# Optimization experiments

Measured on AMD Instinct MI355X. Metric: run time of the kernel, lower is better.

The kernel has to match this reference:

```python
import jax, jax.numpy as jnp
import numpy as np

E = 1024      # emb_size == hidden_size
H = 8         # n_heads
BATCH = 8
NUM = 48      # table rows
KW = 48       # table columns (keys)
L = NUM * KW  # 2304


def _mha(q_in, kv_in, length, Wq, bq, Wk, bk, Wv, bv, Wo, bo, n_heads=H):
    # q_in: (B, T, E), kv_in: (B, S, E); returns (T, B, E) per the torch layout.
    B, T, Em = q_in.shape
    S = kv_in.shape[1]
    dh = Em // n_heads
    q = (q_in @ Wq + bq).reshape(B, T, n_heads, dh).transpose(0, 2, 1, 3)
    k = (kv_in @ Wk + bk).reshape(B, S, n_heads, dh).transpose(0, 2, 1, 3)
    v = (kv_in @ Wv + bv).reshape(B, S, n_heads, dh).transpose(0, 2, 1, 3)
    scores = jnp.einsum('bhtd,bhsd->bhts', q, k) / jnp.asarray(np.sqrt(dh), q.dtype)
    mask = jnp.arange(S) < length  # memory_lengths masking
    scores = jnp.where(mask[None, None, None, :], scores, jnp.finfo(scores.dtype).min)
    attn = jax.nn.softmax(scores, axis=-1)
    out = jnp.einsum('bhts,bhsd->bhtd', attn, v).transpose(0, 2, 1, 3).reshape(B, T, Em)
    out = out @ Wo + bo
    return out.transpose(1, 0, 2)  # (T, B, E)


def setup_inputs() -> dict:
    key = jax.random.key(0)
    ks = jax.random.split(key, 24)

    def W(k, shape, s=0.03):
        return jax.random.normal(k, shape, dtype=jnp.float32) * s

    inp = {
        'emb': jax.random.normal(ks[0], (L, BATCH, E), dtype=jnp.float32),
        # col attention params
        'Wq_c': W(ks[1], (E, E)), 'bq_c': jnp.zeros((E,), jnp.float32),
        'Wk_c': W(ks[2], (E, E)), 'bk_c': jnp.zeros((E,), jnp.float32),
        'Wv_c': W(ks[3], (E, E)), 'bv_c': jnp.zeros((E,), jnp.float32),
        'Wo_c': W(ks[4], (E, E)), 'bo_c': jnp.zeros((E,), jnp.float32),
        # row attention params
        'Wq_r': W(ks[5], (E, E)), 'bq_r': jnp.zeros((E,), jnp.float32),
        'Wk_r': W(ks[6], (E, E)), 'bk_r': jnp.zeros((E,), jnp.float32),
        'Wv_r': W(ks[7], (E, E)), 'bv_r': jnp.zeros((E,), jnp.float32),
        'Wo_r': W(ks[8], (E, E)), 'bo_r': jnp.zeros((E,), jnp.float32),
        # fusion layers
        'W_gen': W(ks[9], (2 * E, E)),
        'W_mlp1': W(ks[10], (2 * E, E)),
        'W_mlp2': W(ks[11], (E, 1)),
        # scalar forward args
        'start_id': 0, 'end_id': L - 1,
        'num': NUM, 'num_tensor': NUM,
        'kw_num': KW, 'kw_num_tensor': KW,
        'batch': BATCH,
    }
    return inp


def reference(emb, Wq_c, bq_c, Wk_c, bk_c, Wv_c, bv_c, Wo_c, bo_c,
              Wq_r, bq_r, Wk_r, bk_r, Wv_r, bv_r, Wo_r, bo_r,
              W_gen, W_mlp1, W_mlp2,
              start_id, end_id, num, num_tensor, kw_num, kw_num_tensor, batch):
    Em = emb.shape[-1]
    length = end_id - start_id + 1  # = num * kw_num
    # emb.narrow(0, start_id, length): (L, batch, E)
    rep = emb[start_id:start_id + length]
    # -> (kw_num, batch*num, E)
    home_ply_rep = rep.transpose(1, 0, 2).reshape(batch * num, kw_num, Em).transpose(1, 0, 2)

    # --- column-dim encoding: attention over the `num` (row) axis ---
    col_mb = jnp.swapaxes(home_ply_rep.reshape(kw_num, batch, num, Em), 0, 2)  # (num, batch, kw, E)
    col_mb = col_mb.reshape(num, batch * kw_num, Em)
    col_q = col_mb.transpose(1, 0, 2)  # (batch*kw, num, E)
    col_rep = _mha(col_q, col_q, num_tensor, Wq_c, bq_c, Wk_c, bk_c, Wv_c, bv_c, Wo_c, bo_c)
    # (num, batch*kw, E) -> (kw_num, batch*num, E)
    col_dim_rep = jnp.swapaxes(col_rep.reshape(num, batch, kw_num, Em), 0, 2).reshape(kw_num, batch * num, Em)

    # --- row-dim encoding: attention over the `kw_num` (column) axis ---
    row_q = col_dim_rep.transpose(1, 0, 2)  # (batch*num, kw, E)
    row_dim_rep = _mha(row_q, row_q, kw_num_tensor, Wq_r, bq_r, Wk_r, bk_r, Wv_r, bv_r, Wo_r, bo_r)  # (kw, b*n, E)

    # --- fusion: concat + Linear + tanh, MLP scores, softmax over {row, col} ---
    gen_rep = jnp.tanh(jnp.concatenate([row_dim_rep, col_dim_rep], axis=-1) @ W_gen)

    def mlp_score(x):
        return jnp.tanh(jnp.concatenate([x, gen_rep], axis=-1) @ W_mlp1) @ W_mlp2  # (kw, b*n, 1)

    row_score = mlp_score(row_dim_rep)
    col_score = mlp_score(col_dim_rep)
    w = jax.nn.softmax(jnp.concatenate([row_score, col_score], axis=-1), axis=-1)  # (kw, b*n, 2)
    home_ply_memory_bank = w[..., 0:1] * row_dim_rep + w[..., 1:2] * col_dim_rep
    # no_fusion=True -> residual add
    home_ply_memory_bank = home_ply_memory_bank + home_ply_rep

    row_for_ptr = row_dim_rep.reshape(kw_num, batch, num, Em)
    col_for_ptr = col_dim_rep.reshape(kw_num, batch, num, Em)

    # row_aggregation == 'mean'
    home_ply_row_rep = home_ply_memory_bank.mean(axis=0)  # (batch*num, E)
    home_ply_row_rep = home_ply_row_rep.reshape(batch, num, Em).transpose(1, 0, 2)  # (num, batch, E)
    return (home_ply_row_rep, home_ply_memory_bank, col_for_ptr, row_for_ptr)
```

## Files before the change

kernel.cpp:

```cpp
#include <hip/hip_runtime.h>
#include <hip/hip_bf16.h>
#include <stdint.h>

typedef unsigned short u16;
typedef unsigned int   u32;
typedef __attribute__((ext_vector_type(4))) float f32x4;
typedef __attribute__((ext_vector_type(2))) float f32x2;
typedef __attribute__((ext_vector_type(8))) short s16x8;

#define DEV __device__ __forceinline__

static constexpr int EDIM  = 1024;
static constexpr int MROWS = 8 * 48 * 48;
static constexpr int MT256 = MROWS / 256;

DEV float b2f(u16 x) { u32 u = ((u32)x) << 16; float f; __builtin_memcpy(&f, &u, 4); return f; }
DEV u16 f2b(float f) {
    u32 u; __builtin_memcpy(&u, &f, 4);
    u32 r = (u + 0x7FFFu + ((u >> 16) & 1u)) >> 16;
    return (u16)r;
}

#define GLDS16(gsrc, ldst) __builtin_amdgcn_global_load_lds( \
    (const __attribute__((address_space(1))) u32*)(gsrc),    \
    (__attribute__((address_space(3))) u32*)(ldst), 16, 0, 0)

#define BAR()   __builtin_amdgcn_s_barrier()
#define LGKM0() asm volatile("s_waitcnt lgkmcnt(0)" ::: "memory")

__global__ void wconv_kernel(const float* __restrict__ W, u16* __restrict__ Wt,
                             int K, int N) {
    __shared__ u16 tile[64][65];
    int n0 = blockIdx.x * 64, k0 = blockIdx.y * 64;
    int tx = threadIdx.x & 63, ty = threadIdx.x >> 6;
#pragma unroll
    for (int i = 0; i < 16; ++i) {
        int r = ty * 16 + i;
        tile[r][tx] = f2b(W[(size_t)(k0 + r) * N + n0 + tx]);
    }
    __syncthreads();
#pragma unroll
    for (int i = 0; i < 16; ++i) {
        int r = ty * 16 + i;
        Wt[(size_t)(n0 + r) * K + k0 + tx] = tile[tx][r];
    }
}

__global__ void bconcat_kernel(const float* __restrict__ a, const float* __restrict__ b,
                               const float* __restrict__ c, float* __restrict__ out) {
    int i = blockIdx.x * 256 + threadIdx.x;
    out[i] = (i < 1024) ? a[i] : ((i < 2048) ? b[i - 1024] : c[i - 2048]);
}

__global__ void gather_kernel(const float* __restrict__ emb, u16* __restrict__ Xc) {
    int gid = blockIdx.x * 256 + threadIdx.x;
    int r = gid >> 9, c2 = gid & 511;
    int b = r / 2304, k = (r / 48) % 48, n = r % 48;
    int src = (n * 48 + k) * 8 + b;
    f32x2 v = *(const f32x2*)&emb[(size_t)src * EDIM + c2 * 2];
    u32 p = (u32)f2b(v.x) | ((u32)f2b(v.y) << 16);
    *(u32*)&Xc[(size_t)r * EDIM + c2 * 2] = p;
}

__global__ void zero_kernel(float* __restrict__ p, int n) {
    int i = blockIdx.x * 256 + threadIdx.x;
    if (i < n) p[i] = 0.f;
}

DEV s16x8 ldsrd(const u16* lds, int r, int kk, int qq) {
    int gl = kk * 4 + qq;
    return *(const s16x8*)&lds[r * 64 + ((gl ^ (r & 7)) << 3)];
}

DEV void stage_tileA(u16* lds, const u16* Ag, int lda, int m0, int ka,
                     int h, int wv, int lane) {
#pragma unroll
    for (int i = 0; i < 2; ++i) {
        int blk  = wv * 2 + i;
        int row0 = (h + 2 * (blk >> 3)) * 64 + (blk & 7) * 8;
        int rr   = row0 + (lane >> 3);
        int gl   = (lane & 7) ^ (rr & 7);
        const u16* g = Ag + (size_t)(m0 + rr) * lda + ka + gl * 8;
        GLDS16(g, lds + row0 * 64);
    }
}

DEV void stage_tileB(u16* lds, const u16* Bg, int ldb, int n0, int kb,
                     int h, int wv, int lane) {
#pragma unroll
    for (int i = 0; i < 2; ++i) {
        int blk  = wv * 2 + i;
        int row0 = (blk >> 2) * 64 + h * 32 + (blk & 3) * 8;
        int rr   = row0 + (lane >> 3);
        int gl   = (lane & 7) ^ (rr & 7);
        const u16* g = Bg + (size_t)(n0 + rr) * ldb + kb + gl * 8;
        GLDS16(g, lds + row0 * 64);
    }
}

template<int KTOT, bool DUALA, bool TANH, bool PERM, bool SCORE, bool WRC, int OMAP, bool MERGE2>
__global__ __launch_bounds__(512, 2) void gemm256_kernel(
    const u16* __restrict__ A1, const u16* __restrict__ A1b,
    const u16* __restrict__ A2, int lda,
    const u16* __restrict__ Bt, const float* __restrict__ bias,
    u16* __restrict__ C, int ldc, float* __restrict__ outF,
    const float* __restrict__ w2, float* __restrict__ score,
    float* __restrict__ scoreb) {
    __shared__ u16 lA[2][256 * 64];
    __shared__ u16 lB[2][256 * 64];
    constexpr int NT = KTOT / 64;

    int bid = blockIdx.x;
    if (MERGE2 && bid >= MT256 * 4) { bid -= MT256 * 4; A1 = A1b; score = scoreb; }
    int mt = bid % MT256, nt = bid / MT256;
    int m0 = mt * 256, n0 = nt * 256;
    int tid = threadIdx.x, lane = tid & 63, wv = tid >> 6;
    int wm = wv >> 2, wn = wv & 3;
    int fr = lane & 15, qq = lane >> 4;

    auto Asel = [&](int ts, const u16*& Ag, int& ka) {
        ka = ts * 64; Ag = A1;
        if (DUALA && ka >= 1024) { Ag = A2; ka -= 1024; }
    };

    f32x4 acc[8][4];
#pragma unroll
    for (int i = 0; i < 8; ++i)
#pragma unroll
        for (int j = 0; j < 4; ++j) acc[i][j] = (f32x4)0.f;

    {
        const u16* Ag; int ka; Asel(0, Ag, ka);
        stage_tileA(&lA[0][0], Ag, lda, m0, ka, 0, wv, lane);
        stage_tileA(&lA[0][0], Ag, lda, m0, ka, 1, wv, lane);
        stage_tileB(&lB[0][0], Bt, KTOT, n0, 0, 0, wv, lane);
        stage_tileB(&lB[0][0], Bt, KTOT, n0, 0, 1, wv, lane);
    }
    if (NT > 1) {
        const u16* Ag; int ka; Asel(1, Ag, ka);
        stage_tileA(&lA[1][0], Ag, lda, m0, ka, 0, wv, lane);
        stage_tileB(&lB[1][0], Bt, KTOT, n0, 64, 0, wv, lane);
        stage_tileB(&lB[1][0], Bt, KTOT, n0, 64, 1, wv, lane);
    }
    asm volatile("s_waitcnt vmcnt(6)" ::: "memory");
    BAR();

    s16x8 A8[8], B0[4], B1[4];

    for (int t = 0; t < NT; ++t) {
        int buf = t & 1;
        const u16* lAb = &lA[buf][0];
        const u16* lBb = &lB[buf][0];

#pragma unroll
        for (int m = 0; m < 4; ++m)
#pragma unroll
            for (int kk = 0; kk < 2; ++kk)
                A8[m * 2 + kk] = ldsrd(lAb, wm * 128 + m * 16 + fr, kk, qq);
#pragma unroll
        for (int n = 0; n < 2; ++n)
#pragma unroll
            for (int kk = 0; kk < 2; ++kk)
                B0[n * 2 + kk] = ldsrd(lBb, wn * 64 + n * 16 + fr, kk, qq);
        if (t + 1 < NT) {
            const u16* Ag; int ka; Asel(t + 1, Ag, ka);
            stage_tileA(&lA[buf ^ 1][0], Ag, lda, m0, ka, 1, wv, lane);
        }
        BAR(); LGKM0();
        __builtin_amdgcn_s_setprio(1);
#pragma unroll
        for (int m = 0; m < 4; ++m)
#pragma unroll
            for (int n = 0; n < 2; ++n)
#pragma unroll
                for (int kk = 0; kk < 2; ++kk)
                    acc[m][n] = __builtin_amdgcn_mfma_f32_16x16x32_bf16(
                        A8[m * 2 + kk], B0[n * 2 + kk], acc[m][n], 0, 0, 0);
        __builtin_amdgcn_s_setprio(0);
        BAR();

#pragma unroll
        for (int n = 0; n < 2; ++n)
#pragma unroll
            for (int kk = 0; kk < 2; ++kk)
                B1[n * 2 + kk] = ldsrd(lBb, wn * 64 + 32 + n * 16 + fr, kk, qq);
        if (t + 2 < NT) {
            const u16* Ag; int ka; Asel(t + 2, Ag, ka);
            stage_tileA(&lA[buf][0], Ag, lda, m0, ka, 0, wv, lane);
        }
        BAR(); LGKM0();
        __builtin_amdgcn_s_setprio(1);
#pragma unroll
        for (int m = 0; m < 4; ++m)
#pragma unroll
            for (int n = 0; n < 2; ++n)
#pragma unroll
                for (int kk = 0; kk < 2; ++kk)
                    acc[m][n + 2] = __builtin_amdgcn_mfma_f32_16x16x32_bf16(
                        A8[m * 2 + kk], B1[n * 2 + kk], acc[m][n + 2], 0, 0, 0);
        __builtin_amdgcn_s_setprio(0);
        BAR();

#pragma unroll
        for (int m = 0; m < 4; ++m)
#pragma unroll
            for (int kk = 0; kk < 2; ++kk)
                A8[m * 2 + kk] = ldsrd(lAb, wm * 128 + 64 + m * 16 + fr, kk, qq);
        if (t + 2 < NT)
            stage_tileB(&lB[buf][0], Bt, KTOT, n0, (t + 2) * 64, 0, wv, lane);
        BAR(); LGKM0();
        __builtin_amdgcn_s_setprio(1);
#pragma unroll
        for (int m = 0; m < 4; ++m)
#pragma unroll
            for (int n = 0; n < 2; ++n)
#pragma unroll
                for (int kk = 0; kk < 2; ++kk)
                    acc[m + 4][n] = __builtin_amdgcn_mfma_f32_16x16x32_bf16(
                        A8[m * 2 + kk], B0[n * 2 + kk], acc[m + 4][n], 0, 0, 0);
        __builtin_amdgcn_s_setprio(0);
        BAR();

        if (t + 2 < NT)
            stage_tileB(&lB[buf][0], Bt, KTOT, n0, (t + 2) * 64, 1, wv, lane);
        __builtin_amdgcn_s_setprio(1);
#pragma unroll
        for (int m = 0; m < 4; ++m)
#pragma unroll
            for (int n = 0; n < 2; ++n)
#pragma unroll
                for (int kk = 0; kk < 2; ++kk)
                    acc[m + 4][n + 2] = __builtin_amdgcn_mfma_f32_16x16x32_bf16(
                        A8[m * 2 + kk], B1[n * 2 + kk], acc[m + 4][n + 2], 0, 0, 0);
        __builtin_amdgcn_s_setprio(0);
        if (t < NT - 2)       asm volatile("s_waitcnt vmcnt(6)" ::: "memory");
        else if (t == NT - 2) asm volatile("s_waitcnt vmcnt(0)" ::: "memory");
        BAR();
    }

    int crow4 = qq * 4;
#pragma unroll
    for (int mf = 0; mf < 8; ++mf) {
#pragma unroll
        for (int j = 0; j < 4; ++j) {
            int row = m0 + wm * 128 + mf * 16 + crow4 + j;
            int orow = row;
            int o32 = 0;
            if (PERM || OMAP == 1) {
                int b = row / 2304, k = (row / 48) % 48, n = row % 48;
                if (PERM) orow = (b * 48 + n) * 48 + k;
                if (OMAP == 1) o32 = k * 384 + b * 48 + n;
            }
            if (OMAP == 2) {
                int b = row / 2304, n = (row / 48) % 48, k = row % 48;
                o32 = k * 384 + b * 48 + n;
            }
            float sc_part = 0.f;
#pragma unroll
            for (int nf = 0; nf < 4; ++nf) {
                int col = n0 + wn * 64 + nf * 16 + fr;
                float v = acc[mf][nf][j];
                if (bias) v += bias[col];
                if (TANH) v = tanhf(v);
                if (WRC) C[(size_t)orow * ldc + col] = f2b(v);
                if (OMAP) outF[(size_t)o32 * EDIM + col] = v;
                if (SCORE) sc_part += v * w2[col];
            }
            if (SCORE) {
                sc_part += __shfl_xor(sc_part, 1);
                sc_part += __shfl_xor(sc_part, 2);
                sc_part += __shfl_xor(sc_part, 4);
                sc_part += __shfl_xor(sc_part, 8);
                if (fr == 0) atomicAdd(&score[row], sc_part);
            }
        }
    }
}

__global__ __launch_bounds__(64) void attn_kernel(u16* __restrict__ QKV) {
    __shared__ u16 lVt[128 * 72];
    __shared__ u16 lP[48 * 72];
    const int LDQ = 3072;
    int bb = blockIdx.x >> 3, h = blockIdx.x & 7;
    int lane = threadIdx.x;
    u16* Qp = QKV + (size_t)bb * 48 * LDQ + h * 128;
    const u16* Kp = Qp + 1024;
    const u16* Vp = Qp + 2048;

#pragma unroll
    for (int i = 0; i < 48; ++i) {
        u32 vv = *(const u32*)&Vp[(size_t)i * LDQ + lane * 2];
        lVt[(lane * 2) * 72 + i]     = (u16)(vv & 0xffffu);
        lVt[(lane * 2 + 1) * 72 + i] = (u16)(vv >> 16);
    }
    for (int i = lane; i < 128 * 16; i += 64) { int d = i >> 4, c = 48 + (i & 15); lVt[d * 72 + c] = 0; }
    for (int i = lane; i < 48 * 16; i += 64)  { int t = i >> 4, c = 48 + (i & 15); lP[t * 72 + c] = 0; }
    __syncthreads();

    int fr = lane & 15, fk = (lane >> 4) * 8, crow4 = (lane >> 4) * 4;
    f32x4 sc[3][3];
#pragma unroll
    for (int mf = 0; mf < 3; ++mf)
#pragma unroll
        for (int nf = 0; nf < 3; ++nf) sc[mf][nf] = (f32x4)0.f;

#pragma unroll
    for (int kk = 0; kk < 4; ++kk) {
        s16x8 aq[3], bk[3];
#pragma unroll
        for (int mf = 0; mf < 3; ++mf) aq[mf] = *(const s16x8*)&Qp[(size_t)(mf * 16 + fr) * LDQ + kk * 32 + fk];
#pragma unroll
        for (int nf = 0; nf < 3; ++nf) bk[nf] = *(const s16x8*)&Kp[(size_t)(nf * 16 + fr) * LDQ + kk * 32 + fk];
#pragma unroll
        for (int mf = 0; mf < 3; ++mf)
#pragma unroll
            for (int nf = 0; nf < 3; ++nf)
                sc[mf][nf] = __builtin_amdgcn_mfma_f32_16x16x32_bf16(aq[mf], bk[nf], sc[mf][nf], 0, 0, 0);
    }

    const float scale = 0.08838834764831845f;
#pragma unroll
    for (int mf = 0; mf < 3; ++mf) {
#pragma unroll
        for (int j = 0; j < 4; ++j) {
            float v0 = sc[mf][0][j] * scale;
            float v1 = sc[mf][1][j] * scale;
            float v2 = sc[mf][2][j] * scale;
            float mx = fmaxf(v0, fmaxf(v1, v2));
            mx = fmaxf(mx, __shfl_xor(mx, 1));
            mx = fmaxf(mx, __shfl_xor(mx, 2));
            mx = fmaxf(mx, __shfl_xor(mx, 4));
            mx = fmaxf(mx, __shfl_xor(mx, 8));
            float e0 = __expf(v0 - mx), e1 = __expf(v1 - mx), e2 = __expf(v2 - mx);
            float s = e0 + e1 + e2;
            s += __shfl_xor(s, 1);
            s += __shfl_xor(s, 2);
            s += __shfl_xor(s, 4);
            s += __shfl_xor(s, 8);
            float inv = 1.f / s;
            int t = mf * 16 + crow4 + j;
            lP[t * 72 + 0  + fr] = f2b(e0 * inv);
            lP[t * 72 + 16 + fr] = f2b(e1 * inv);
            lP[t * 72 + 32 + fr] = f2b(e2 * inv);
        }
    }
    __syncthreads();

    f32x4 o[3][8];
#pragma unroll
    for (int mf = 0; mf < 3; ++mf)
#pragma unroll
        for (int nf = 0; nf < 8; ++nf) o[mf][nf] = (f32x4)0.f;

#pragma unroll
    for (int kk = 0; kk < 2; ++kk) {
        s16x8 ap[3];
#pragma unroll
        for (int mf = 0; mf < 3; ++mf) ap[mf] = *(const s16x8*)&lP[(mf * 16 + fr) * 72 + kk * 32 + fk];
#pragma unroll
        for (int nf = 0; nf < 8; ++nf) {
            s16x8 bv = *(const s16x8*)&lVt[(nf * 16 + fr) * 72 + kk * 32 + fk];
#pragma unroll
            for (int mf = 0; mf < 3; ++mf)
                o[mf][nf] = __builtin_amdgcn_mfma_f32_16x16x32_bf16(ap[mf], bv, o[mf][nf], 0, 0, 0);
        }
    }
#pragma unroll
    for (int mf = 0; mf < 3; ++mf)
#pragma unroll
        for (int nf = 0; nf < 8; ++nf)
#pragma unroll
            for (int j = 0; j < 4; ++j) {
                int t = mf * 16 + crow4 + j, d = nf * 16 + fr;
                Qp[(size_t)t * LDQ + d] = f2b(o[mf][nf][j]);
            }
}

__global__ void combine_kernel(const u16* __restrict__ RDR, const u16* __restrict__ CDR,
                               const float* __restrict__ srow, const float* __restrict__ scol,
                               const float* __restrict__ emb, float* __restrict__ out_mb) {
    int o = blockIdx.x;
    int k = o / 384, b = (o / 48) & 7, n = o % 48;
    int r2 = (b * 48 + n) * 48 + k;
    float rs = srow[r2], cs = scol[r2];
    float m = fmaxf(rs, cs);
    float e0 = __expf(rs - m), e1 = __expf(cs - m);
    float inv = 1.f / (e0 + e1);
    float w0 = e0 * inv, w1 = e1 * inv;
    const size_t rb = (size_t)r2 * EDIM;
    const size_t ob = (size_t)o * EDIM;
    const size_t eb = ((size_t)(n * 48 + k) * 8 + b) * EDIM;
    for (int e = threadIdx.x; e < EDIM; e += 256) {
        float rv = b2f(RDR[rb + e]);
        float cv = b2f(CDR[rb + e]);
        out_mb[ob + e] = w0 * rv + w1 * cv + emb[eb + e];
    }
}

__global__ void mean_kernel(const float* __restrict__ mb, float* __restrict__ out0) {
    int idx = blockIdx.x * 256 + threadIdx.x;
    int n = idx >> 13, b = (idx >> 10) & 7, e = idx & 1023;
    float s = 0.f;
#pragma unroll 8
    for (int k = 0; k < 48; ++k) s += mb[((size_t)(k * 384 + b * 48 + n)) * EDIM + e];
    out0[idx] = s * (1.f / 48.f);
}

extern "C" void kernel_launch(void* const* d_in, const int* in_sizes, int n_in,
                              void* d_out, int out_size, void* d_ws, size_t ws_size,
                              hipStream_t stream) {
    const float* emb    = (const float*)d_in[0];
    const float* Wq_c   = (const float*)d_in[1];
    const float* bq_c   = (const float*)d_in[2];
    const float* Wk_c   = (const float*)d_in[3];
    const float* bk_c   = (const float*)d_in[4];
    const float* Wv_c   = (const float*)d_in[5];
    const float* bv_c   = (const float*)d_in[6];
    const float* Wo_c   = (const float*)d_in[7];
    const float* bo_c   = (const float*)d_in[8];
    const float* Wq_r   = (const float*)d_in[9];
    const float* bq_r   = (const float*)d_in[10];
    const float* Wk_r   = (const float*)d_in[11];
    const float* bk_r   = (const float*)d_in[12];
    const float* Wv_r   = (const float*)d_in[13];
    const float* bv_r   = (const float*)d_in[14];
    const float* Wo_r   = (const float*)d_in[15];
    const float* bo_r   = (const float*)d_in[16];
    const float* W_gen  = (const float*)d_in[17];
    const float* W_mlp1 = (const float*)d_in[18];
    const float* W_mlp2 = (const float*)d_in[19];

    char* ws = (char*)d_ws;
    size_t off = 0;
    auto alloc = [&](size_t bytes) { char* p = ws + off; off += (bytes + 255) & ~(size_t)255; return p; };
    u16*   WqkvC = (u16*)alloc((size_t)3072 * 1024 * 2);
    u16*   WqkvR = (u16*)alloc((size_t)3072 * 1024 * 2);
    u16*   WoC   = (u16*)alloc((size_t)1024 * 1024 * 2);
    u16*   WoR   = (u16*)alloc((size_t)1024 * 1024 * 2);
    u16*   WgT   = (u16*)alloc((size_t)1024 * 2048 * 2);
    u16*   W1T   = (u16*)alloc((size_t)1024 * 2048 * 2);
    float* bqkvC = (float*)alloc(3072 * 4);
    float* bqkvR = (float*)alloc(3072 * 4);
    u16*   XA    = (u16*)alloc((size_t)MROWS * 1024 * 2);
    u16*   QKV   = (u16*)alloc((size_t)MROWS * 3072 * 2);
    u16*   CDR   = (u16*)alloc((size_t)MROWS * 1024 * 2);
    u16*   RDR   = (u16*)alloc((size_t)MROWS * 1024 * 2);
    float* score_row = (float*)alloc((size_t)MROWS * 4);
    float* score_col = (float*)alloc((size_t)MROWS * 4);
    (void)ws_size; (void)in_sizes; (void)n_in; (void)out_size;

    dim3 tb(256);
    wconv_kernel<<<dim3(16, 16), tb, 0, stream>>>(Wq_c, WqkvC,                   1024, 1024);
    wconv_kernel<<<dim3(16, 16), tb, 0, stream>>>(Wk_c, WqkvC + 1024 * 1024,     1024, 1024);
    wconv_kernel<<<dim3(16, 16), tb, 0, stream>>>(Wv_c, WqkvC + 2 * 1024 * 1024, 1024, 1024);
    wconv_kernel<<<dim3(16, 16), tb, 0, stream>>>(Wo_c, WoC,                     1024, 1024);
    wconv_kernel<<<dim3(16, 16), tb, 0, stream>>>(Wq_r, WqkvR,                   1024, 1024);
    wconv_kernel<<<dim3(16, 16), tb, 0, stream>>>(Wk_r, WqkvR + 1024 * 1024,     1024, 1024);
    wconv_kernel<<<dim3(16, 16), tb, 0, stream>>>(Wv_r, WqkvR + 2 * 1024 * 1024, 1024, 1024);
    wconv_kernel<<<dim3(16, 16), tb, 0, stream>>>(Wo_r, WoR,                     1024, 1024);
    wconv_kernel<<<dim3(16, 32), tb, 0, stream>>>(W_gen,  WgT, 2048, 1024);
    wconv_kernel<<<dim3(16, 32), tb, 0, stream>>>(W_mlp1, W1T, 2048, 1024);
    bconcat_kernel<<<12, tb, 0, stream>>>(bq_c, bk_c, bv_c, bqkvC);
    bconcat_kernel<<<12, tb, 0, stream>>>(bq_r, bk_r, bv_r, bqkvR);

    gather_kernel<<<MROWS * 512 / 256, tb, 0, stream>>>(emb, XA);
    zero_kernel<<<(2 * MROWS + 255) / 256, tb, 0, stream>>>(score_row, 2 * MROWS);

    float* out = (float*)d_out;
    float* out_mb  = out + 393216;
    float* out_col = out + 393216 + 18874368;
    float* out_row = out + 393216 + 2 * 18874368;

    dim3 tb512(512);
    const int G12 = MT256 * 12, G4 = MT256 * 4, G8m = MT256 * 8;
    gemm256_kernel<1024, false, false, false, false, true, 0, false><<<G12, tb512, 0, stream>>>(
        XA, nullptr, nullptr, 1024, WqkvC, bqkvC, QKV, 3072, nullptr, nullptr, nullptr, nullptr);
    attn_kernel<<<384 * 8, 64, 0, stream>>>(QKV);
    gemm256_kernel<1024, false, false, true, false, true, 1, false><<<G4, tb512, 0, stream>>>(
        QKV, nullptr, nullptr, 3072, WoC, bo_c, CDR, 1024, out_col, nullptr, nullptr, nullptr);
    gemm256_kernel<1024, false, false, false, false, true, 0, false><<<G12, tb512, 0, stream>>>(
        CDR, nullptr, nullptr, 1024, WqkvR, bqkvR, QKV, 3072, nullptr, nullptr, nullptr, nullptr);
    attn_kernel<<<384 * 8, 64, 0, stream>>>(QKV);
    gemm256_kernel<1024, false, false, false, false, true, 2, false><<<G4, tb512, 0, stream>>>(
        QKV, nullptr, nullptr, 3072, WoR, bo_r, RDR, 1024, out_row, nullptr, nullptr, nullptr);
    gemm256_kernel<2048, true, true, false, false, true, 0, false><<<G4, tb512, 0, stream>>>(
        RDR, nullptr, CDR, 1024, WgT, nullptr, XA, 1024, nullptr, nullptr, nullptr, nullptr);
    gemm256_kernel<2048, true, true, false, true, false, 0, true><<<G8m, tb512, 0, stream>>>(
        RDR, CDR, XA, 1024, W1T, nullptr, nullptr, 1024, nullptr, W_mlp2, score_row, score_col);

    combine_kernel<<<MROWS, tb, 0, stream>>>(RDR, CDR, score_row, score_col, emb, out_mb);
    mean_kernel<<<393216 / 256, tb, 0, stream>>>(out_mb, out);
}
```

Baseline: 1.203 ms.

## Fold output projections into downstream weights and persist GEMM tiles across jobs

Precomputes the products of the column-attention output projection with the row QKV weights, and of the row output projection with the first half of the gen weights, including folded biases. The row QKV projection and the gen GEMM can then read the attention outputs directly and run alongside the output-projection GEMMs in one persistent multi-job GEMM launch. The GEMM becomes a persistent 256-block kernel that prefetches the next tile's K-slices across tile boundaries and drops some barriers. Weight conversions, bias concatenation and score zeroing are batched into fewer launches, and combine plus mean are fused. The extra weight-product GEMMs run on every call, and products formed in bf16 add rounding error.

Measured after the change: 1.319 ms. +9.7%, slower.

```diff
diff --git a/kernel.cpp b/kernel.cpp
--- a/kernel.cpp
+++ b/kernel.cpp
@@ -12,7 +12,6 @@
 
 static constexpr int EDIM  = 1024;
 static constexpr int MROWS = 8 * 48 * 48;
-static constexpr int MT256 = MROWS / 256;
 
 DEV float b2f(u16 x) { u32 u = ((u32)x) << 16; float f; __builtin_memcpy(&f, &u, 4); return f; }
 DEV u16 f2b(float f) {
@@ -28,28 +27,89 @@
 #define BAR()   __builtin_amdgcn_s_barrier()
 #define LGKM0() asm volatile("s_waitcnt lgkmcnt(0)" ::: "memory")
 
-__global__ void wconv_kernel(const float* __restrict__ W, u16* __restrict__ Wt,
-                             int K, int N) {
+enum { F_WRC = 1, F_PERM = 2, F_TANH = 4, F_SCORE = 8, F_OMAP1 = 16, F_OMAP2 = 32 };
+
+struct GJob {
+    const u16* A1; const u16* A2; const u16* Bt; const float* bias;
+    u16* C; float* outF; const float* w2; float* score;
+    int lda, lda2, ldc, KTOT, M, flags, tileEnd, pad;
+};
+struct GSet { int njobs, total; GJob j[2]; };
+
+struct WJob { const float* src; u16* dst; int srcN, dstLd, kOff, nT, tileEnd, pad; };
+struct WSet { int n, total; WJob j[11]; };
+
+__global__ void wconvJ_kernel(WSet ws) {
+    int bid = blockIdx.x;
+    int ji = 0;
+    while (bid >= ws.j[ji].tileEnd) ++ji;
+    int base = ji ? ws.j[ji - 1].tileEnd : 0;
+    WJob J = ws.j[ji];
+    int lt = bid - base;
+    int n0 = (lt % J.nT) * 64, k0 = (lt / J.nT) * 64;
     __shared__ u16 tile[64][65];
-    int n0 = blockIdx.x * 64, k0 = blockIdx.y * 64;
     int tx = threadIdx.x & 63, ty = threadIdx.x >> 6;
 #pragma unroll
     for (int i = 0; i < 16; ++i) {
         int r = ty * 16 + i;
-        tile[r][tx] = f2b(W[(size_t)(k0 + r) * N + n0 + tx]);
+        tile[r][tx] = f2b(J.src[(size_t)(k0 + r) * J.srcN + n0 + tx]);
     }
     __syncthreads();
 #pragma unroll
     for (int i = 0; i < 16; ++i) {
         int r = ty * 16 + i;
-        Wt[(size_t)(n0 + r) * K + k0 + tx] = tile[tx][r];
-    }
-}
-
-__global__ void bconcat_kernel(const float* __restrict__ a, const float* __restrict__ b,
-                               const float* __restrict__ c, float* __restrict__ out) {
-    int i = blockIdx.x * 256 + threadIdx.x;
-    out[i] = (i < 1024) ? a[i] : ((i < 2048) ? b[i - 1024] : c[i - 2048]);
+        J.dst[(size_t)(n0 + r) * J.dstLd + J.kOff + k0 + tx] = tile[tx][r];
+    }
+}
+
+__global__ void misc_kernel(const float* WoCsrc, const float* WoRsrc,
+                            u16* WoCnt, u16* WoRnt,
+                            const float* bq_c, const float* bk_c, const float* bv_c, float* bqkvC,
+                            const float* bq_r, const float* bk_r, const float* bv_r,
+                            const float* bo_c, const u16* WqkvRT, float* bqkvR_eff,
+                            const float* bo_r, const u16* WgaT, float* bgen_lin,
+                            float* scores) {
+    int id = blockIdx.x * 256 + threadIdx.x;
+    const int C1 = 1024 * 1024 / 2;
+    if (id < C1) {
+        f32x2 v = *(const f32x2*)&WoCsrc[(size_t)id * 2];
+        *(u32*)&WoCnt[(size_t)id * 2] = (u32)f2b(v.x) | ((u32)f2b(v.y) << 16);
+        return;
+    }
+    id -= C1;
+    if (id < C1) {
+        f32x2 v = *(const f32x2*)&WoRsrc[(size_t)id * 2];
+        *(u32*)&WoRnt[(size_t)id * 2] = (u32)f2b(v.x) | ((u32)f2b(v.y) << 16);
+        return;
+    }
+    id -= C1;
+    if (id < 3072) { bqkvC[id] = (id < 1024) ? bq_c[id] : (id < 2048) ? bk_c[id - 1024] : bv_c[id - 2048]; return; }
+    id -= 3072;
+    if (id < 2 * MROWS) { scores[id] = 0.f; return; }
+    id -= 2 * MROWS;
+    if (id < 3072) {
+        float s = (id < 1024) ? bq_r[id] : (id < 2048) ? bk_r[id - 1024] : bv_r[id - 2048];
+        float d = 0.f;
+        const u16* row = &WqkvRT[(size_t)id * 1024];
+        for (int e = 0; e < 1024; e += 8) {
+            s16x8 v = *(const s16x8*)&row[e];
+#pragma unroll
+            for (int u = 0; u < 8; ++u) d += bo_c[e + u] * b2f((u16)v[u]);
+        }
+        bqkvR_eff[id] = s + d;
+        return;
+    }
+    id -= 3072;
+    if (id < 1024) {
+        float d = 0.f;
+        const u16* row = &WgaT[(size_t)id * 1024];
+        for (int e = 0; e < 1024; e += 8) {
+            s16x8 v = *(const s16x8*)&row[e];
+#pragma unroll
+            for (int u = 0; u < 8; ++u) d += bo_r[e + u] * b2f((u16)v[u]);
+        }
+        bgen_lin[id] = d;
+    }
 }
 
 __global__ void gather_kernel(const float* __restrict__ emb, u16* __restrict__ Xc) {
@@ -58,97 +118,91 @@
     int b = r / 2304, k = (r / 48) % 48, n = r % 48;
     int src = (n * 48 + k) * 8 + b;
     f32x2 v = *(const f32x2*)&emb[(size_t)src * EDIM + c2 * 2];
-    u32 p = (u32)f2b(v.x) | ((u32)f2b(v.y) << 16);
-    *(u32*)&Xc[(size_t)r * EDIM + c2 * 2] = p;
-}
-
-__global__ void zero_kernel(float* __restrict__ p, int n) {
-    int i = blockIdx.x * 256 + threadIdx.x;
-    if (i < n) p[i] = 0.f;
+    *(u32*)&Xc[(size_t)r * EDIM + c2 * 2] = (u32)f2b(v.x) | ((u32)f2b(v.y) << 16);
 }
 
 DEV s16x8 ldsrd(const u16* lds, int r, int kk, int qq) {
     int gl = kk * 4 + qq;
     return *(const s16x8*)&lds[r * 64 + ((gl ^ (r & 7)) << 3)];
 }
-
-DEV void stage_tileA(u16* lds, const u16* Ag, int lda, int m0, int ka,
-                     int h, int wv, int lane) {
+DEV void stageA_p(u16* lds, const u16* Ag, int lda, int m0, int ka, int h, int wv, int lane) {
 #pragma unroll
     for (int i = 0; i < 2; ++i) {
-        int blk  = wv * 2 + i;
+        int blk = wv * 2 + i;
         int row0 = (h + 2 * (blk >> 3)) * 64 + (blk & 7) * 8;
-        int rr   = row0 + (lane >> 3);
-        int gl   = (lane & 7) ^ (rr & 7);
-        const u16* g = Ag + (size_t)(m0 + rr) * lda + ka + gl * 8;
-        GLDS16(g, lds + row0 * 64);
-    }
-}
-
-DEV void stage_tileB(u16* lds, const u16* Bg, int ldb, int n0, int kb,
-                     int h, int wv, int lane) {
+        int rr = row0 + (lane >> 3);
+        int gl = (lane & 7) ^ (rr & 7);
+        GLDS16(Ag + (size_t)(m0 + rr) * lda + ka + gl * 8, lds + row0 * 64);
+    }
+}
+DEV void stageB_p(u16* lds, const u16* Bg, int ldb, int n0, int kb, int h, int wv, int lane) {
 #pragma unroll
     for (int i = 0; i < 2; ++i) {
-        int blk  = wv * 2 + i;
+        int blk = wv * 2 + i;
         int row0 = (blk >> 2) * 64 + h * 32 + (blk & 3) * 8;
-        int rr   = row0 + (lane >> 3);
-        int gl   = (lane & 7) ^ (rr & 7);
-        const u16* g = Bg + (size_t)(n0 + rr) * ldb + kb + gl * 8;
-        GLDS16(g, lds + row0 * 64);
-    }
-}
-
-template<int KTOT, bool DUALA, bool TANH, bool PERM, bool SCORE, bool WRC, int OMAP, bool MERGE2>
-__global__ __launch_bounds__(512, 2) void gemm256_kernel(
-    const u16* __restrict__ A1, const u16* __restrict__ A1b,
-    const u16* __restrict__ A2, int lda,
-    const u16* __restrict__ Bt, const float* __restrict__ bias,
-    u16* __restrict__ C, int ldc, float* __restrict__ outF,
-    const float* __restrict__ w2, float* __restrict__ score,
-    float* __restrict__ scoreb) {
+        int rr = row0 + (lane >> 3);
+        int gl = (lane & 7) ^ (rr & 7);
+        GLDS16(Bg + (size_t)(n0 + rr) * ldb + kb + gl * 8, lds + row0 * 64);
+    }
+}
+
+__global__ __launch_bounds__(512, 2) void gemmP_kernel(GSet js) {
     __shared__ u16 lA[2][256 * 64];
     __shared__ u16 lB[2][256 * 64];
-    constexpr int NT = KTOT / 64;
-
-    int bid = blockIdx.x;
-    if (MERGE2 && bid >= MT256 * 4) { bid -= MT256 * 4; A1 = A1b; score = scoreb; }
-    int mt = bid % MT256, nt = bid / MT256;
-    int m0 = mt * 256, n0 = nt * 256;
     int tid = threadIdx.x, lane = tid & 63, wv = tid >> 6;
     int wm = wv >> 2, wn = wv & 3;
     int fr = lane & 15, qq = lane >> 4;
-
-    auto Asel = [&](int ts, const u16*& Ag, int& ka) {
-        ka = ts * 64; Ag = A1;
-        if (DUALA && ka >= 1024) { Ag = A2; ka -= 1024; }
+    int G = gridDim.x;
+    int tIdx = blockIdx.x;
+    if (tIdx >= js.total) return;
+
+    int cm0, cn0, cNT, cji, nm0, nn0, nNT, nji;
+    bool hasN;
+    auto resolve = [&](int ti, int& m0, int& n0, int& NT, int& ji) {
+        int j = (js.njobs > 1 && ti >= js.j[0].tileEnd) ? 1 : 0;
+        int lt = ti - (j ? js.j[0].tileEnd : 0);
+        int mtl = js.j[j].M >> 8;
+        m0 = (lt % mtl) * 256; n0 = (lt / mtl) * 256;
+        NT = js.j[j].KTOT >> 6; ji = j;
     };
+    resolve(tIdx, cm0, cn0, cNT, cji);
+    int tN = tIdx + G;
+    hasN = tN < js.total;
+    if (hasN) resolve(tN, nm0, nn0, nNT, nji);
+
+    auto stA = [&](int dstbuf, int td, int h) -> bool {
+        const GJob* J; int m0, kk;
+        if (td < cNT) { J = &js.j[cji]; m0 = cm0; kk = td * 64; }
+        else { int u = td - cNT; if (!hasN || u >= nNT) return false;
+               J = &js.j[nji]; m0 = nm0; kk = u * 64; }
+        const u16* Ag = J->A1; int lda = J->lda;
+        if (J->A2 && kk >= 1024) { Ag = J->A2; lda = J->lda2; kk -= 1024; }
+        stageA_p(&lA[dstbuf][0], Ag, lda, m0, kk, h, wv, lane);
+        return true;
+    };
+    auto stB = [&](int dstbuf, int td, int h) -> bool {
+        const GJob* J; int n0, kk;
+        if (td < cNT) { J = &js.j[cji]; n0 = cn0; kk = td * 64; }
+        else { int u = td - cNT; if (!hasN || u >= nNT) return false;
+               J = &js.j[nji]; n0 = nn0; kk = u * 64; }
+        stageB_p(&lB[dstbuf][0], J->Bt, J->KTOT, n0, kk, h, wv, lane);
+        return true;
+    };
 
     f32x4 acc[8][4];
 #pragma unroll
     for (int i = 0; i < 8; ++i)
 #pragma unroll
-        for (int j = 0; j < 4; ++j) acc[i][j] = (f32x4)0.f;
-
-    {
-        const u16* Ag; int ka; Asel(0, Ag, ka);
-        stage_tileA(&lA[0][0], Ag, lda, m0, ka, 0, wv, lane);
-        stage_tileA(&lA[0][0], Ag, lda, m0, ka, 1, wv, lane);
-        stage_tileB(&lB[0][0], Bt, KTOT, n0, 0, 0, wv, lane);
-        stage_tileB(&lB[0][0], Bt, KTOT, n0, 0, 1, wv, lane);
-    }
-    if (NT > 1) {
-        const u16* Ag; int ka; Asel(1, Ag, ka);
-        stage_tileA(&lA[1][0], Ag, lda, m0, ka, 0, wv, lane);
-        stage_tileB(&lB[1][0], Bt, KTOT, n0, 64, 0, wv, lane);
-        stage_tileB(&lB[1][0], Bt, KTOT, n0, 64, 1, wv, lane);
-    }
+        for (int jj = 0; jj < 4; ++jj) acc[i][jj] = (f32x4)0.f;
+
+    stA(0, 0, 0); stA(0, 0, 1); stB(0, 0, 0); stB(0, 0, 1);
+    stA(1, 1, 0); stB(1, 1, 0); stB(1, 1, 1);
     asm volatile("s_waitcnt vmcnt(6)" ::: "memory");
     BAR();
 
     s16x8 A8[8], B0[4], B1[4];
-
-    for (int t = 0; t < NT; ++t) {
-        int buf = t & 1;
+    int buf = 0, t = 0;
+    for (;;) {
         const u16* lAb = &lA[buf][0];
         const u16* lBb = &lB[buf][0];
 
@@ -162,11 +216,8 @@
 #pragma unroll
             for (int kk = 0; kk < 2; ++kk)
                 B0[n * 2 + kk] = ldsrd(lBb, wn * 64 + n * 16 + fr, kk, qq);
-        if (t + 1 < NT) {
-            const u16* Ag; int ka; Asel(t + 1, Ag, ka);
-            stage_tileA(&lA[buf ^ 1][0], Ag, lda, m0, ka, 1, wv, lane);
-        }
-        BAR(); LGKM0();
+        bool h1ex = stA(buf ^ 1, t + 1, 1);
+        LGKM0();
         __builtin_amdgcn_s_setprio(1);
 #pragma unroll
         for (int m = 0; m < 4; ++m)
@@ -184,11 +235,8 @@
 #pragma unroll
             for (int kk = 0; kk < 2; ++kk)
                 B1[n * 2 + kk] = ldsrd(lBb, wn * 64 + 32 + n * 16 + fr, kk, qq);
-        if (t + 2 < NT) {
-            const u16* Ag; int ka; Asel(t + 2, Ag, ka);
-            stage_tileA(&lA[buf][0], Ag, lda, m0, ka, 0, wv, lane);
-        }
-        BAR(); LGKM0();
+        bool h2ex = stA(buf, t + 2, 0);
+        LGKM0();
         __builtin_amdgcn_s_setprio(1);
 #pragma unroll
         for (int m = 0; m < 4; ++m)
@@ -206,9 +254,8 @@
 #pragma unroll
             for (int kk = 0; kk < 2; ++kk)
                 A8[m * 2 + kk] = ldsrd(lAb, wm * 128 + 64 + m * 16 + fr, kk, qq);
-        if (t + 2 < NT)
-            stage_tileB(&lB[buf][0], Bt, KTOT, n0, (t + 2) * 64, 0, wv, lane);
-        BAR(); LGKM0();
+        stB(buf, t + 2, 0);
+        LGKM0();
         __builtin_amdgcn_s_setprio(1);
 #pragma unroll
         for (int m = 0; m < 4; ++m)
@@ -221,8 +268,7 @@
         __builtin_amdgcn_s_setprio(0);
         BAR();
 
-        if (t + 2 < NT)
-            stage_tileB(&lB[buf][0], Bt, KTOT, n0, (t + 2) * 64, 1, wv, lane);
+        stB(buf, t + 2, 1);
         __builtin_amdgcn_s_setprio(1);
 #pragma unroll
         for (int m = 0; m < 4; ++m)
@@ -233,46 +279,59 @@
                     acc[m + 4][n + 2] = __builtin_amdgcn_mfma_f32_16x16x32_bf16(
                         A8[m * 2 + kk], B1[n * 2 + kk], acc[m + 4][n + 2], 0, 0, 0);
         __builtin_amdgcn_s_setprio(0);
-        if (t < NT - 2)       asm volatile("s_waitcnt vmcnt(6)" ::: "memory");
-        else if (t == NT - 2) asm volatile("s_waitcnt vmcnt(0)" ::: "memory");
+        if (h2ex)      asm volatile("s_waitcnt vmcnt(6)" ::: "memory");
+        else if (h1ex) asm volatile("s_waitcnt vmcnt(0)" ::: "memory");
         BAR();
-    }
-
-    int crow4 = qq * 4;
-#pragma unroll
-    for (int mf = 0; mf < 8; ++mf) {
-#pragma unroll
-        for (int j = 0; j < 4; ++j) {
-            int row = m0 + wm * 128 + mf * 16 + crow4 + j;
-            int orow = row;
-            int o32 = 0;
-            if (PERM || OMAP == 1) {
-                int b = row / 2304, k = (row / 48) % 48, n = row % 48;
-                if (PERM) orow = (b * 48 + n) * 48 + k;
-                if (OMAP == 1) o32 = k * 384 + b * 48 + n;
+
+        buf ^= 1; ++t;
+        if (t == cNT) {
+            GJob J = js.j[cji];
+            int crow4 = qq * 4;
+#pragma unroll
+            for (int mf = 0; mf < 8; ++mf) {
+#pragma unroll
+                for (int jj = 0; jj < 4; ++jj) {
+                    int row = cm0 + wm * 128 + mf * 16 + crow4 + jj;
+                    int orow = row, o32 = 0;
+                    if (J.flags & (F_PERM | F_OMAP1)) {
+                        int b = row / 2304, k = (row / 48) % 48, n = row % 48;
+                        if (J.flags & F_PERM)  orow = (b * 48 + n) * 48 + k;
+                        if (J.flags & F_OMAP1) o32 = k * 384 + b * 48 + n;
+                    }
+                    if (J.flags & F_OMAP2) {
+                        int b = row / 2304, n = (row / 48) % 48, k = row % 48;
+                        o32 = k * 384 + b * 48 + n;
+                    }
+                    float sc = 0.f;
+#pragma unroll
+                    for (int nf = 0; nf < 4; ++nf) {
+                        int col = cn0 + wn * 64 + nf * 16 + fr;
+                        float v = acc[mf][nf][jj];
+                        if (J.bias) v += J.bias[col];
+                        if (J.flags & F_TANH) v = tanhf(v);
+                        if (J.flags & F_WRC) J.C[(size_t)orow * J.ldc + col] = f2b(v);
+                        if (J.flags & (F_OMAP1 | F_OMAP2)) J.outF[(size_t)o32 * EDIM + col] = v;
+                        if (J.flags & F_SCORE) sc += v * J.w2[col];
+                    }
+                    if (J.flags & F_SCORE) {
+                        sc += __shfl_xor(sc, 1);
+                        sc += __shfl_xor(sc, 2);
+                        sc += __shfl_xor(sc, 4);
+                        sc += __shfl_xor(sc, 8);
+                        if (fr == 0) atomicAdd(&J.score[row], sc);
+                    }
+                }
             }
-            if (OMAP == 2) {
-                int b = row / 2304, n = (row / 48) % 48, k = row % 48;
-                o32 = k * 384 + b * 48 + n;
-            }
-            float sc_part = 0.f;
-#pragma unroll
-            for (int nf = 0; nf < 4; ++nf) {
-                int col = n0 + wn * 64 + nf * 16 + fr;
-                float v = acc[mf][nf][j];
-                if (bias) v += bias[col];
-                if (TANH) v = tanhf(v);
-                if (WRC) C[(size_t)orow * ldc + col] = f2b(v);
-                if (OMAP) outF[(size_t)o32 * EDIM + col] = v;
-                if (SCORE) sc_part += v * w2[col];
-            }
-            if (SCORE) {
-                sc_part += __shfl_xor(sc_part, 1);
-                sc_part += __shfl_xor(sc_part, 2);
-                sc_part += __shfl_xor(sc_part, 4);
-                sc_part += __shfl_xor(sc_part, 8);
-                if (fr == 0) atomicAdd(&score[row], sc_part);
-            }
+            if (!hasN) break;
+#pragma unroll
+            for (int i = 0; i < 8; ++i)
+#pragma unroll
+                for (int jj = 0; jj < 4; ++jj) acc[i][jj] = (f32x4)0.f;
+            cm0 = nm0; cn0 = nn0; cNT = nNT; cji = nji;
+            tN += G;
+            hasN = tN < js.total;
+            if (hasN) resolve(tN, nm0, nn0, nNT, nji);
+            t = 0;
         }
     }
 }
@@ -376,34 +435,35 @@
             }
 }
 
-__global__ void combine_kernel(const u16* __restrict__ RDR, const u16* __restrict__ CDR,
-                               const float* __restrict__ srow, const float* __restrict__ scol,
-                               const float* __restrict__ emb, float* __restrict__ out_mb) {
-    int o = blockIdx.x;
-    int k = o / 384, b = (o / 48) & 7, n = o % 48;
-    int r2 = (b * 48 + n) * 48 + k;
-    float rs = srow[r2], cs = scol[r2];
-    float m = fmaxf(rs, cs);
-    float e0 = __expf(rs - m), e1 = __expf(cs - m);
-    float inv = 1.f / (e0 + e1);
-    float w0 = e0 * inv, w1 = e1 * inv;
-    const size_t rb = (size_t)r2 * EDIM;
-    const size_t ob = (size_t)o * EDIM;
-    const size_t eb = ((size_t)(n * 48 + k) * 8 + b) * EDIM;
-    for (int e = threadIdx.x; e < EDIM; e += 256) {
-        float rv = b2f(RDR[rb + e]);
-        float cv = b2f(CDR[rb + e]);
-        out_mb[ob + e] = w0 * rv + w1 * cv + emb[eb + e];
-    }
-}
-
-__global__ void mean_kernel(const float* __restrict__ mb, float* __restrict__ out0) {
-    int idx = blockIdx.x * 256 + threadIdx.x;
-    int n = idx >> 13, b = (idx >> 10) & 7, e = idx & 1023;
-    float s = 0.f;
-#pragma unroll 8
-    for (int k = 0; k < 48; ++k) s += mb[((size_t)(k * 384 + b * 48 + n)) * EDIM + e];
-    out0[idx] = s * (1.f / 48.f);
+__global__ void combine_mean_kernel(const u16* __restrict__ RDR, const u16* __restrict__ CDR,
+                                    const float* __restrict__ srow, const float* __restrict__ scol,
+                                    const float* __restrict__ emb, float* __restrict__ out) {
+    int b = blockIdx.x / 48, n = blockIdx.x % 48;
+    __shared__ float w0s[48], w1s[48];
+    int tx = threadIdx.x;
+    if (tx < 48) {
+        int r2 = (b * 48 + n) * 48 + tx;
+        float rs = srow[r2], cs = scol[r2];
+        float m = fmaxf(rs, cs);
+        float e0 = __expf(rs - m), e1 = __expf(cs - m);
+        float inv = 1.f / (e0 + e1);
+        w0s[tx] = e0 * inv; w1s[tx] = e1 * inv;
+    }
+    __syncthreads();
+    float* out_mb = out + 393216;
+    for (int e = tx; e < EDIM; e += 256) {
+        float s = 0.f;
+        for (int k = 0; k < 48; ++k) {
+            size_t rb = (size_t)((b * 48 + n) * 48 + k) * EDIM;
+            float rv = b2f(RDR[rb + e]);
+            float cv = b2f(CDR[rb + e]);
+            float hv = emb[((size_t)(n * 48 + k) * 8 + b) * EDIM + e];
+            float v = w0s[k] * rv + w1s[k] * cv + hv;
+            out_mb[(size_t)(k * 384 + b * 48 + n) * EDIM + e] = v;
+            s += v;
+        }
+        out[(size_t)(n * 8 + b) * EDIM + e] = s * (1.f / 48.f);
+    }
 }
 
 extern "C" void kernel_launch(void* const* d_in, const int* in_sizes, int n_in,
@@ -429,65 +489,112 @@
     const float* W_gen  = (const float*)d_in[17];
     const float* W_mlp1 = (const float*)d_in[18];
     const float* W_mlp2 = (const float*)d_in[19];
+    (void)in_sizes; (void)n_in; (void)out_size; (void)ws_size;
 
     char* ws = (char*)d_ws;
     size_t off = 0;
     auto alloc = [&](size_t bytes) { char* p = ws + off; off += (bytes + 255) & ~(size_t)255; return p; };
-    u16*   WqkvC = (u16*)alloc((size_t)3072 * 1024 * 2);
-    u16*   WqkvR = (u16*)alloc((size_t)3072 * 1024 * 2);
-    u16*   WoC   = (u16*)alloc((size_t)1024 * 1024 * 2);
-    u16*   WoR   = (u16*)alloc((size_t)1024 * 1024 * 2);
-    u16*   WgT   = (u16*)alloc((size_t)1024 * 2048 * 2);
-    u16*   W1T   = (u16*)alloc((size_t)1024 * 2048 * 2);
-    float* bqkvC = (float*)alloc(3072 * 4);
-    float* bqkvR = (float*)alloc(3072 * 4);
-    u16*   XA    = (u16*)alloc((size_t)MROWS * 1024 * 2);
-    u16*   QKV   = (u16*)alloc((size_t)MROWS * 3072 * 2);
-    u16*   CDR   = (u16*)alloc((size_t)MROWS * 1024 * 2);
-    u16*   RDR   = (u16*)alloc((size_t)MROWS * 1024 * 2);
+    u16*   WqkvCT = (u16*)alloc((size_t)3072 * 1024 * 2);
+    u16*   WqkvRT = (u16*)alloc((size_t)3072 * 1024 * 2);
+    u16*   WoCT   = (u16*)alloc((size_t)1024 * 1024 * 2);
+    u16*   WoRT   = (u16*)alloc((size_t)1024 * 1024 * 2);
+    u16*   WoCnt  = (u16*)alloc((size_t)1024 * 1024 * 2);
+    u16*   WoRnt  = (u16*)alloc((size_t)1024 * 1024 * 2);
+    u16*   WgaT   = (u16*)alloc((size_t)1024 * 1024 * 2);
+    u16*   BtGf   = (u16*)alloc((size_t)1024 * 2048 * 2);
+    u16*   W1T    = (u16*)alloc((size_t)1024 * 2048 * 2);
+    u16*   BtQKVr = (u16*)alloc((size_t)3072 * 1024 * 2);
+    float* bqkvC  = (float*)alloc(3072 * 4);
+    float* bqkvRe = (float*)alloc(3072 * 4);
+    float* bgen   = (float*)alloc(1024 * 4);
+    u16*   XA     = (u16*)alloc((size_t)MROWS * 1024 * 2);
+    u16*   QKV    = (u16*)alloc((size_t)MROWS * 3072 * 2);
+    u16*   QKV2   = (u16*)alloc((size_t)MROWS * 3072 * 2);
+    u16*   CDR    = (u16*)alloc((size_t)MROWS * 1024 * 2);
+    u16*   RDR    = (u16*)alloc((size_t)MROWS * 1024 * 2);
     float* score_row = (float*)alloc((size_t)MROWS * 4);
     float* score_col = (float*)alloc((size_t)MROWS * 4);
-    (void)ws_size; (void)in_sizes; (void)n_in; (void)out_size;
-
-    dim3 tb(256);
-    wconv_kernel<<<dim3(16, 16), tb, 0, stream>>>(Wq_c, WqkvC,                   1024, 1024);
-    wconv_kernel<<<dim3(16, 16), tb, 0, stream>>>(Wk_c, WqkvC + 1024 * 1024,     1024, 1024);
-    wconv_kernel<<<dim3(16, 16), tb, 0, stream>>>(Wv_c, WqkvC + 2 * 1024 * 1024, 1024, 1024);
-    wconv_kernel<<<dim3(16, 16), tb, 0, stream>>>(Wo_c, WoC,                     1024, 1024);
-    wconv_kernel<<<dim3(16, 16), tb, 0, stream>>>(Wq_r, WqkvR,                   1024, 1024);
-    wconv_kernel<<<dim3(16, 16), tb, 0, stream>>>(Wk_r, WqkvR + 1024 * 1024,     1024, 1024);
-    wconv_kernel<<<dim3(16, 16), tb, 0, stream>>>(Wv_r, WqkvR + 2 * 1024 * 1024, 1024, 1024);
-    wconv_kernel<<<dim3(16, 16), tb, 0, stream>>>(Wo_r, WoR,                     1024, 1024);
-    wconv_kernel<<<dim3(16, 32), tb, 0, stream>>>(W_gen,  WgT, 2048, 1024);
-    wconv_kernel<<<dim3(16, 32), tb, 0, stream>>>(W_mlp1, W1T, 2048, 1024);
-    bconcat_kernel<<<12, tb, 0, stream>>>(bq_c, bk_c, bv_c, bqkvC);
-    bconcat_kernel<<<12, tb, 0, stream>>>(bq_r, bk_r, bv_r, bqkvR);
-
-    gather_kernel<<<MROWS * 512 / 256, tb, 0, stream>>>(emb, XA);
-    zero_kernel<<<(2 * MROWS + 255) / 256, tb, 0, stream>>>(score_row, 2 * MROWS);
 
     float* out = (float*)d_out;
-    float* out_mb  = out + 393216;
     float* out_col = out + 393216 + 18874368;
     float* out_row = out + 393216 + 2 * 18874368;
 
-    dim3 tb512(512);
-    const int G12 = MT256 * 12, G4 = MT256 * 4, G8m = MT256 * 8;
-    gemm256_kernel<1024, false, false, false, false, true, 0, false><<<G12, tb512, 0, stream>>>(
-        XA, nullptr, nullptr, 1024, WqkvC, bqkvC, QKV, 3072, nullptr, nullptr, nullptr, nullptr);
+    dim3 tb(256), tb512(512);
+
+    WSet wset = {};
+    int te = 0;
+    auto addW = [&](const float* src, u16* dst, int srcN, int dstLd, int kOff, int nT, int kT) {
+        int i = wset.n++;
+        te += nT * kT;
+        WJob w = {src, dst, srcN, dstLd, kOff, nT, te, 0};
+        wset.j[i] = w;
+    };
+    addW(Wq_c, WqkvCT,                   1024, 1024, 0, 16, 16);
+    addW(Wk_c, WqkvCT + 1024 * 1024,     1024, 1024, 0, 16, 16);
+    addW(Wv_c, WqkvCT + 2 * 1024 * 1024, 1024, 1024, 0, 16, 16);
+    addW(Wo_c, WoCT,                     1024, 1024, 0, 16, 16);
+    addW(Wq_r, WqkvRT,                   1024, 1024, 0, 16, 16);
+    addW(Wk_r, WqkvRT + 1024 * 1024,     1024, 1024, 0, 16, 16);
+    addW(Wv_r, WqkvRT + 2 * 1024 * 1024, 1024, 1024, 0, 16, 16);
+    addW(Wo_r, WoRT,                     1024, 1024, 0, 16, 16);
+    addW(W_gen,               WgaT,      1024, 1024, 0, 16, 16);
+    addW(W_gen + 1024 * 1024, BtGf,      1024, 2048, 1024, 16, 16);
+    addW(W_mlp1,              W1T,       1024, 2048, 0, 16, 32);
+    wset.total = te;
+    wconvJ_kernel<<<te, tb, 0, stream>>>(wset);
+
+    int miscItems = 1024 * 1024 + 3072 + 2 * MROWS + 3072 + 1024;
+    misc_kernel<<<(miscItems + 255) / 256, tb, 0, stream>>>(
+        Wo_c, Wo_r, WoCnt, WoRnt,
+        bq_c, bk_c, bv_c, bqkvC,
+        bq_r, bk_r, bv_r,
+        bo_c, WqkvRT, bqkvRe,
+        bo_r, WgaT, bgen,
+        score_row);
+
+    gather_kernel<<<MROWS * 512 / 256, tb, 0, stream>>>(emb, XA);
+
+    auto mkJob = [](const u16* A1, const u16* A2, const u16* Bt, const float* bias,
+                    u16* C, float* outF, const float* w2, float* score,
+                    int lda, int lda2, int ldc, int KTOT, int M, int flags) {
+        GJob j = {A1, A2, Bt, bias, C, outF, w2, score, lda, lda2, ldc, KTOT, M, flags, 0, 0};
+        return j;
+    };
+    auto run1 = [&](GJob a, int nA) {
+        GSet gs = {};
+        a.tileEnd = (a.M >> 8) * nA;
+        gs.njobs = 1; gs.total = a.tileEnd; gs.j[0] = a;
+        gemmP_kernel<<<256, tb512, 0, stream>>>(gs);
+    };
+    auto run2 = [&](GJob a, int nA, GJob b, int nB) {
+        GSet gs = {};
+        a.tileEnd = (a.M >> 8) * nA;
+        b.tileEnd = a.tileEnd + (b.M >> 8) * nB;
+        gs.njobs = 2; gs.total = b.tileEnd; gs.j[0] = a; gs.j[1] = b;
+        gemmP_kernel<<<256, tb512, 0, stream>>>(gs);
+    };
+
+    run2(mkJob(WqkvRT, nullptr, WoCnt, nullptr, BtQKVr, nullptr, nullptr, nullptr,
+               1024, 0, 1024, 1024, 3072, F_WRC), 4,
+         mkJob(WgaT, nullptr, WoRnt, nullptr, BtGf, nullptr, nullptr, nullptr,
+               1024, 0, 2048, 1024, 1024, F_WRC), 4);
+
+    run1(mkJob(XA, nullptr, WqkvCT, bqkvC, QKV, nullptr, nullptr, nullptr,
+               1024, 0, 3072, 1024, MROWS, F_WRC), 12);
     attn_kernel<<<384 * 8, 64, 0, stream>>>(QKV);
-    gemm256_kernel<1024, false, false, true, false, true, 1, false><<<G4, tb512, 0, stream>>>(
-        QKV, nullptr, nullptr, 3072, WoC, bo_c, CDR, 1024, out_col, nullptr, nullptr, nullptr);
-    gemm256_kernel<1024, false, false, false, false, true, 0, false><<<G12, tb512, 0, stream>>>(
-        CDR, nullptr, nullptr, 1024, WqkvR, bqkvR, QKV, 3072, nullptr, nullptr, nullptr, nullptr);
-    attn_kernel<<<384 * 8, 64, 0, stream>>>(QKV);
-    gemm256_kernel<1024, false, false, false, false, true, 2, false><<<G4, tb512, 0, stream>>>(
-        QKV, nullptr, nullptr, 3072, WoR, bo_r, RDR, 1024, out_row, nullptr, nullptr, nullptr);
-    gemm256_kernel<2048, true, true, false, false, true, 0, false><<<G4, tb512, 0, stream>>>(
-        RDR, nullptr, CDR, 1024, WgT, nullptr, XA, 1024, nullptr, nullptr, nullptr, nullptr);
-    gemm256_kernel<2048, true, true, false, true, false, 0, true><<<G8m, tb512, 0, stream>>>(
-        RDR, CDR, XA, 1024, W1T, nullptr, nullptr, 1024, nullptr, W_mlp2, score_row, score_col);
-
-    combine_kernel<<<MROWS, tb, 0, stream>>>(RDR, CDR, score_row, score_col, emb, out_mb);
-    mean_kernel<<<393216 / 256, tb, 0, stream>>>(out_mb, out);
-}
+    run2(mkJob(QKV, nullptr, WoCT, bo_c, CDR, out_col, nullptr, nullptr,
+               3072, 0, 1024, 1024, MROWS, F_WRC | F_PERM | F_OMAP1), 4,
+         mkJob(QKV, nullptr, BtQKVr, bqkvRe, QKV2, nullptr, nullptr, nullptr,
+               3072, 0, 3072, 1024, MROWS, F_WRC | F_PERM), 12);
+    attn_kernel<<<384 * 8, 64, 0, stream>>>(QKV2);
+    run2(mkJob(QKV2, nullptr, WoRT, bo_r, RDR, out_row, nullptr, nullptr,
+               3072, 0, 1024, 1024, MROWS, F_WRC | F_OMAP2), 4,
+         mkJob(QKV2, CDR, BtGf, bgen, XA, nullptr, nullptr, nullptr,
+               3072, 1024, 1024, 2048, MROWS, F_WRC | F_TANH), 4);
+    run2(mkJob(RDR, XA, W1T, nullptr, nullptr, nullptr, W_mlp2, score_row,
+               1024, 1024, 1024, 2048, MROWS, F_SCORE | F_TANH), 4,
+         mkJob(CDR, XA, W1T, nullptr, nullptr, nullptr, W_mlp2, score_col,
+               1024, 1024, 1024, 2048, MROWS, F_SCORE | F_TANH), 4);
+
+    combine_mean_kernel<<<384, tb, 0, stream>>>(RDR, CDR, score_row, score_col, emb, out);
+}
```
